# Optimization experiments

Measured on AMD Instinct MI355X. Metric: run time of the kernel, lower is better.

## Reference

```python
import jax, jax.numpy as jnp
import numpy as np

B, C, H, W = 4, 32, 512, 512


def _warp_add(x, flow, residual):
    # x: [B,C,H,W], flow: [B,2,H,W], residual: [B,C,H,W]
    Bs, Cs, Hs, Ws = x.shape
    # align_corners=False pixel-center base grid in [-1,1]
    gy = (jnp.arange(Hs, dtype=x.dtype) + 0.5) * (2.0 / Hs) - 1.0  # [H]
    gx = (jnp.arange(Ws, dtype=x.dtype) + 0.5) * (2.0 / Ws) - 1.0  # [W]
    grid_x = gx[None, None, :] + flow[:, 0]  # [B,H,W]
    grid_y = gy[None, :, None] + flow[:, 1]  # [B,H,W]
    # circular wrap on x only
    grid_x = jnp.mod(grid_x + 1.0, 2.0) - 1.0
    real_x = (grid_x + 1.0) * (Ws * 0.5) - 0.5
    real_y = (grid_y + 1.0) * (Hs * 0.5) - 0.5
    x0 = jnp.floor(real_x)
    y0 = jnp.floor(real_y)
    dx = real_x - x0
    dy = real_y - y0
    ix0 = x0.astype(jnp.int32)
    iy0 = y0.astype(jnp.int32)
    ix1 = ix0 + 1
    iy1 = iy0 + 1

    def valid(ix, iy):
        return (ix >= 0) & (ix < Ws) & (iy >= 0) & (iy < Hs)

    xf = x.reshape(Bs, Cs, Hs * Ws)

    def gather(ix, iy):
        v = valid(ix, iy)  # [B,H,W]
        idx = jnp.clip(iy, 0, Hs - 1) * Ws + jnp.clip(ix, 0, Ws - 1)  # [B,H,W]
        g = jnp.take_along_axis(xf, idx.reshape(Bs, 1, Hs * Ws), axis=2)  # [B,C,H*W]
        g = g.reshape(Bs, Cs, Hs, Ws)
        return jnp.where(v[:, None, :, :], g, 0.0)

    v_tl = gather(ix0, iy0)
    v_tr = gather(ix1, iy0)
    v_bl = gather(ix0, iy1)
    v_br = gather(ix1, iy1)

    w_tl = ((1.0 - dx) * (1.0 - dy))[:, None]
    w_tr = (dx * (1.0 - dy))[:, None]
    w_bl = ((1.0 - dx) * dy)[:, None]
    w_br = (dx * dy)[:, None]

    out = w_tl * v_tl + w_tr * v_tr + w_bl * v_bl + w_br * v_br + residual
    return out


def setup_inputs() -> dict:
    key = jax.random.key(0)
    k1, k2, k3 = jax.random.split(key, 3)
    x = jax.random.normal(k1, (B, C, H, W), dtype=jnp.float32)
    flow = jax.random.normal(k2, (B, 2, H, W), dtype=jnp.float32) * 0.1
    residual = jax.random.normal(k3, (B, C, H, W), dtype=jnp.float32)
    return {"x": x, "flow": flow, "residual": residual}


def reference(x, flow, residual):
    return _warp_add(x, flow, residual)
```

## Files before the change

### kernel.cpp

```cpp
#include <hip/hip_runtime.h>

#define Bdim 4
#define Cdim 32
#define Hdim 512
#define Wdim 512
#define HWdim (Hdim * Wdim)

typedef __attribute__((ext_vector_type(2))) float    f32x2;
typedef __attribute__((ext_vector_type(4))) float    f32x4;
typedef __attribute__((ext_vector_type(2))) _Float16 f16x2;
typedef __attribute__((ext_vector_type(4))) _Float16 f16x4;
typedef __attribute__((ext_vector_type(8))) _Float16 f16x8;

__global__ __launch_bounds__(256) void transpose_nhwc_half_kernel(
    const float* __restrict__ x, _Float16* __restrict__ ws)
{
    __shared__ float lds[Cdim * 65];

    const int idx = blockIdx.x;
    const int tw  = idx & 7;
    const int h   = (idx >> 3) & (Hdim - 1);
    const int b   = idx >> 12;
    const int w0  = tw * 64;

    const int t  = threadIdx.x;
    const int wi = t & 63;
    const int cg = t >> 6;

    #pragma unroll
    for (int i = 0; i < 8; ++i) {
        const int c = cg * 8 + i;
        lds[c * 65 + wi] = x[(((size_t)b * Cdim + c) * Hdim + h) * Wdim + w0 + wi];
    }
    __syncthreads();

    const size_t base = (((size_t)b * Hdim + h) * Wdim + w0) * Cdim;
    const int w_ = t >> 2;
    const int c0 = (t & 3) * 8;
    f16x8 v;
    #pragma unroll
    for (int k = 0; k < 8; ++k) v[k] = (_Float16)lds[(c0 + k) * 65 + w_];
    *(f16x8*)(ws + base + (size_t)t * 8) = v;
}

__global__ __launch_bounds__(256) void gather_nhwc_half_kernel(
    const _Float16* __restrict__ ws,
    const float* __restrict__ flow,
    const float* __restrict__ residual,
    float* __restrict__ out)
{
    __shared__ int      s_off[4][256];
    __shared__ float    s_wt[4][256];
    __shared__ _Float16 s_buf[256 * 34];

    const int idx = blockIdx.x;
    const int b   = idx >> 10;
    const int h   = (idx >> 1) & (Hdim - 1);
    const int w0  = (idx & 1) << 8;
    const int t   = threadIdx.x;

    {
        const int w = w0 + t;
        const int pixg = h * Wdim + w;
        const float fx = flow[((size_t)b * 2 + 0) * HWdim + pixg];
        const float fy = flow[((size_t)b * 2 + 1) * HWdim + pixg];

        float gx = ((float)w + 0.5f) * (2.0f / (float)Wdim) - 1.0f + fx;
        float gy = ((float)h + 0.5f) * (2.0f / (float)Hdim) - 1.0f + fy;

        float tm = fmodf(gx + 1.0f, 2.0f);
        if (tm < 0.0f) tm += 2.0f;
        gx = tm - 1.0f;

        const float real_x = (gx + 1.0f) * ((float)Wdim * 0.5f) - 0.5f;
        const float real_y = (gy + 1.0f) * ((float)Hdim * 0.5f) - 0.5f;

        const float x0f = floorf(real_x);
        const float y0f = floorf(real_y);
        const float dx = real_x - x0f;
        const float dy = real_y - y0f;

        const int ix0 = (int)x0f;
        const int iy0 = (int)y0f;
        const int ix1 = ix0 + 1;
        const int iy1 = iy0 + 1;

        const bool vx0 = (ix0 >= 0) && (ix0 < Wdim);
        const bool vx1 = (ix1 >= 0) && (ix1 < Wdim);
        const bool vy0 = (iy0 >= 0) && (iy0 < Hdim);
        const bool vy1 = (iy1 >= 0) && (iy1 < Hdim);

        const int cx0 = min(max(ix0, 0), Wdim - 1);
        const int cx1 = min(max(ix1, 0), Wdim - 1);
        const int cy0 = min(max(iy0, 0), Hdim - 1);
        const int cy1 = min(max(iy1, 0), Hdim - 1);

        float w_tl = (1.0f - dx) * (1.0f - dy);
        float w_tr = dx * (1.0f - dy);
        float w_bl = (1.0f - dx) * dy;
        float w_br = dx * dy;
        if (!(vx0 && vy0)) w_tl = 0.0f;
        if (!(vx1 && vy0)) w_tr = 0.0f;
        if (!(vx0 && vy1)) w_bl = 0.0f;
        if (!(vx1 && vy1)) w_br = 0.0f;

        s_off[0][t] = (cy0 * Wdim + cx0) * Cdim;
        s_off[1][t] = (cy0 * Wdim + cx1) * Cdim;
        s_off[2][t] = (cy1 * Wdim + cx0) * Cdim;
        s_off[3][t] = (cy1 * Wdim + cx1) * Cdim;
        s_wt[0][t] = w_tl;
        s_wt[1][t] = w_tr;
        s_wt[2][t] = w_bl;
        s_wt[3][t] = w_br;
    }
    __syncthreads();

    {
        const int ci = t & 7;
        const int c0 = ci * 4;
        const int p  = t >> 3;
        const _Float16* xb = ws + (size_t)b * HWdim * Cdim + c0;

        #pragma unroll 4
        for (int j = 0; j < 8; ++j) {
            const int pix = j * 32 + p;
            const int o0 = s_off[0][pix];
            const int o1 = s_off[1][pix];
            const int o2 = s_off[2][pix];
            const int o3 = s_off[3][pix];
            const float w0_ = s_wt[0][pix];
            const float w1_ = s_wt[1][pix];
            const float w2_ = s_wt[2][pix];
            const float w3_ = s_wt[3][pix];

            const f16x4 v0 = *(const f16x4*)(xb + o0);
            const f16x4 v1 = *(const f16x4*)(xb + o1);
            const f16x4 v2 = *(const f16x4*)(xb + o2);
            const f16x4 v3 = *(const f16x4*)(xb + o3);

            float a0 = w0_ * (float)v0[0] + w1_ * (float)v1[0] + w2_ * (float)v2[0] + w3_ * (float)v3[0];
            float a1 = w0_ * (float)v0[1] + w1_ * (float)v1[1] + w2_ * (float)v2[1] + w3_ * (float)v3[1];
            float a2 = w0_ * (float)v0[2] + w1_ * (float)v1[2] + w2_ * (float)v2[2] + w3_ * (float)v3[2];
            float a3 = w0_ * (float)v0[3] + w1_ * (float)v1[3] + w2_ * (float)v2[3] + w3_ * (float)v3[3];

            f16x2 h01; h01[0] = (_Float16)a0; h01[1] = (_Float16)a1;
            f16x2 h23; h23[0] = (_Float16)a2; h23[1] = (_Float16)a3;
            *(f16x2*)(s_buf + pix * 34 + c0)     = h01;
            *(f16x2*)(s_buf + pix * 34 + c0 + 2) = h23;
        }
    }
    __syncthreads();

    {
        const size_t pbase = (size_t)h * Wdim + w0 + t;
        const _Float16* row = s_buf + t * 34;
        #pragma unroll 8
        for (int cc = 0; cc < Cdim; cc += 2) {
            const f16x2 v = *(const f16x2*)(row + cc);
            const size_t gi0 = ((size_t)b * Cdim + cc) * HWdim + pbase;
            const float r0 = __builtin_nontemporal_load(residual + gi0);
            const float r1 = __builtin_nontemporal_load(residual + gi0 + HWdim);
            __builtin_nontemporal_store((float)v[0] + r0, out + gi0);
            __builtin_nontemporal_store((float)v[1] + r1, out + gi0 + HWdim);
        }
    }
}

__global__ __launch_bounds__(256) void warp_add_kernel(
    const float* __restrict__ x,
    const float* __restrict__ flow,
    const float* __restrict__ residual,
    float* __restrict__ out)
{
    int tid = blockIdx.x * blockDim.x + threadIdx.x;
    int w = tid & (Wdim - 1);
    int h = (tid >> 9) & (Hdim - 1);
    int b = tid >> 18;

    const float fx = flow[((size_t)b * 2 + 0) * HWdim + h * Wdim + w];
    const float fy = flow[((size_t)b * 2 + 1) * HWdim + h * Wdim + w];

    float gx = ((float)w + 0.5f) * (2.0f / (float)Wdim) - 1.0f + fx;
    float gy = ((float)h + 0.5f) * (2.0f / (float)Hdim) - 1.0f + fy;
    {
        float t2 = fmodf(gx + 1.0f, 2.0f);
        if (t2 < 0.0f) t2 += 2.0f;
        gx = t2 - 1.0f;
    }
    const float real_x = (gx + 1.0f) * ((float)Wdim * 0.5f) - 0.5f;
    const float real_y = (gy + 1.0f) * ((float)Hdim * 0.5f) - 0.5f;
    const float x0f = floorf(real_x);
    const float y0f = floorf(real_y);
    const float dx = real_x - x0f;
    const float dy = real_y - y0f;
    const int ix0 = (int)x0f, iy0 = (int)y0f;
    const int ix1 = ix0 + 1,  iy1 = iy0 + 1;
    const bool vx0 = (ix0 >= 0) && (ix0 < Wdim);
    const bool vx1 = (ix1 >= 0) && (ix1 < Wdim);
    const bool vy0 = (iy0 >= 0) && (iy0 < Hdim);
    const bool vy1 = (iy1 >= 0) && (iy1 < Hdim);
    const int cx0 = min(max(ix0, 0), Wdim - 1);
    const int cx1 = min(max(ix1, 0), Wdim - 1);
    const int cy0 = min(max(iy0, 0), Hdim - 1);
    const int cy1 = min(max(iy1, 0), Hdim - 1);
    float w_tl = (1.0f - dx) * (1.0f - dy);
    float w_tr = dx * (1.0f - dy);
    float w_bl = (1.0f - dx) * dy;
    float w_br = dx * dy;
    if (!(vx0 && vy0)) w_tl = 0.0f;
    if (!(vx1 && vy0)) w_tr = 0.0f;
    if (!(vx0 && vy1)) w_bl = 0.0f;
    if (!(vx1 && vy1)) w_br = 0.0f;
    const int off_tl = cy0 * Wdim + cx0;
    const int off_tr = cy0 * Wdim + cx1;
    const int off_bl = cy1 * Wdim + cx0;
    const int off_br = cy1 * Wdim + cx1;
    const size_t base = (size_t)b * Cdim * HWdim;
    const int    pix  = h * Wdim + w;
    const float* xb = x + base;
    const float* rb = residual + base + pix;
    float*       ob = out + base + pix;
    #pragma unroll 8
    for (int c = 0; c < Cdim; ++c) {
        const float* xc = xb + (size_t)c * HWdim;
        float v = w_tl * xc[off_tl] + w_tr * xc[off_tr]
                + w_bl * xc[off_bl] + w_br * xc[off_br]
                + rb[(size_t)c * HWdim];
        ob[(size_t)c * HWdim] = v;
    }
}

extern "C" void kernel_launch(void* const* d_in, const int* in_sizes, int n_in,
                              void* d_out, int out_size, void* d_ws, size_t ws_size,
                              hipStream_t stream) {
    const float* x        = (const float*)d_in[0];
    const float* flow     = (const float*)d_in[1];
    const float* residual = (const float*)d_in[2];
    float* out            = (float*)d_out;

    const size_t ws_needed = (size_t)Bdim * Cdim * HWdim * sizeof(_Float16);

    if (ws_size >= ws_needed) {
        _Float16* ws = (_Float16*)d_ws;
        transpose_nhwc_half_kernel<<<Bdim * Hdim * (Wdim / 64), 256, 0, stream>>>(x, ws);
        gather_nhwc_half_kernel<<<Bdim * Hdim * Wdim / 256, 256, 0, stream>>>(ws, flow, residual, out);
    } else {
        const int total = Bdim * Hdim * Wdim;
        warp_add_kernel<<<total / 256, 256, 0, stream>>>(x, flow, residual, out);
    }
}
```

Measured before the change: 349.2 us.

## Widen transpose tiles and batch gather loads with early residual prefetch

The transpose kernel now handles 128-wide tiles and uses float4 global loads, writing two f16x8 chunks per thread. The gather kernel gives each thread 8 channels with f16x8 loads and issues all bilinear corner loads for two pixel batches up front. It also prefetches all 32 residual values into registers before the interpolation math, so gather and residual reads overlap. The cost is much higher register pressure, up to 32 residual floats plus 16 vector loads in flight, which may reduce occupancy.

```diff
diff --git a/kernel.cpp b/kernel.cpp
--- a/kernel.cpp
+++ b/kernel.cpp
@@ -6,7 +6,6 @@
 #define Wdim 512
 #define HWdim (Hdim * Wdim)
 
-typedef __attribute__((ext_vector_type(2))) float    f32x2;
 typedef __attribute__((ext_vector_type(4))) float    f32x4;
 typedef __attribute__((ext_vector_type(2))) _Float16 f16x2;
 typedef __attribute__((ext_vector_type(4))) _Float16 f16x4;
@@ -15,32 +14,40 @@
 __global__ __launch_bounds__(256) void transpose_nhwc_half_kernel(
     const float* __restrict__ x, _Float16* __restrict__ ws)
 {
-    __shared__ float lds[Cdim * 65];
+    __shared__ float lds[Cdim * 132];
 
     const int idx = blockIdx.x;
-    const int tw  = idx & 7;
-    const int h   = (idx >> 3) & (Hdim - 1);
-    const int b   = idx >> 12;
-    const int w0  = tw * 64;
-
-    const int t  = threadIdx.x;
-    const int wi = t & 63;
-    const int cg = t >> 6;
-
-    #pragma unroll
-    for (int i = 0; i < 8; ++i) {
-        const int c = cg * 8 + i;
-        lds[c * 65 + wi] = x[(((size_t)b * Cdim + c) * Hdim + h) * Wdim + w0 + wi];
+    const int tw  = idx & 3;
+    const int h   = (idx >> 2) & (Hdim - 1);
+    const int b   = idx >> 11;
+    const int w0  = tw * 128;
+    const int t   = threadIdx.x;
+
+    f32x4 r[4];
+    #pragma unroll
+    for (int i = 0; i < 4; ++i) {
+        const int f4 = i * 256 + t;
+        const int c  = f4 >> 5;
+        const int w4 = f4 & 31;
+        r[i] = *(const f32x4*)(x + (((size_t)b * Cdim + c) * Hdim + h) * Wdim + w0 + w4 * 4);
+    }
+    #pragma unroll
+    for (int i = 0; i < 4; ++i) {
+        const int f4 = i * 256 + t;
+        *(f32x4*)(lds + (f4 >> 5) * 132 + (f4 & 31) * 4) = r[i];
     }
     __syncthreads();
 
     const size_t base = (((size_t)b * Hdim + h) * Wdim + w0) * Cdim;
-    const int w_ = t >> 2;
-    const int c0 = (t & 3) * 8;
-    f16x8 v;
-    #pragma unroll
-    for (int k = 0; k < 8; ++k) v[k] = (_Float16)lds[(c0 + k) * 65 + w_];
-    *(f16x8*)(ws + base + (size_t)t * 8) = v;
+    const int w_ = t >> 1;
+    const int c0 = (t & 1) * 16;
+    f16x8 v0, v1;
+    #pragma unroll
+    for (int k = 0; k < 8; ++k) v0[k] = (_Float16)lds[(c0 + k) * 132 + w_];
+    #pragma unroll
+    for (int k = 0; k < 8; ++k) v1[k] = (_Float16)lds[(c0 + 8 + k) * 132 + w_];
+    *(f16x8*)(ws + base + (size_t)w_ * Cdim + c0)     = v0;
+    *(f16x8*)(ws + base + (size_t)w_ * Cdim + c0 + 8) = v1;
 }
 
 __global__ __launch_bounds__(256) void gather_nhwc_half_kernel(
@@ -51,7 +58,7 @@
 {
     __shared__ int      s_off[4][256];
     __shared__ float    s_wt[4][256];
-    __shared__ _Float16 s_buf[256 * 34];
+    __shared__ _Float16 s_buf[256 * 36];
 
     const int idx = blockIdx.x;
     const int b   = idx >> 10;
@@ -115,53 +122,83 @@
     }
     __syncthreads();
 
+    const int ci = t & 3;
+    const int c0 = ci * 8;
+    const int p  = t >> 2;
+    const _Float16* xb = ws + (size_t)b * (size_t)HWdim * Cdim + c0;
+    const size_t pbase = (size_t)h * Wdim + w0 + t;
+    const float* rb = residual + (size_t)b * Cdim * (size_t)HWdim + pbase;
+
+    float rres[Cdim];
+
+    int   oa[2][4]; float wa[2][4]; f16x8 va[2][4];
+    #pragma unroll
+    for (int j = 0; j < 2; ++j) {
+        const int pix = j * 64 + p;
+        #pragma unroll
+        for (int k = 0; k < 4; ++k) { oa[j][k] = s_off[k][pix]; wa[j][k] = s_wt[k][pix]; }
+    }
+    #pragma unroll
+    for (int j = 0; j < 2; ++j) {
+        #pragma unroll
+        for (int k = 0; k < 4; ++k) va[j][k] = *(const f16x8*)(xb + (size_t)oa[j][k]);
+    }
+    #pragma unroll
+    for (int c = 0; c < Cdim; ++c) rres[c] = __builtin_nontemporal_load(rb + (size_t)c * HWdim);
+
+    #pragma unroll
+    for (int j = 0; j < 2; ++j) {
+        const int pix = j * 64 + p;
+        float acc[8];
+        #pragma unroll
+        for (int e = 0; e < 8; ++e)
+            acc[e] = wa[j][0] * (float)va[j][0][e] + wa[j][1] * (float)va[j][1][e]
+                   + wa[j][2] * (float)va[j][2][e] + wa[j][3] * (float)va[j][3][e];
+        f16x4 h0, h1;
+        #pragma unroll
+        for (int e = 0; e < 4; ++e) { h0[e] = (_Float16)acc[e]; h1[e] = (_Float16)acc[4 + e]; }
+        *(f16x4*)(s_buf + pix * 36 + c0)     = h0;
+        *(f16x4*)(s_buf + pix * 36 + c0 + 4) = h1;
+    }
+
+    int   ob[2][4]; float wb[2][4]; f16x8 vb[2][4];
+    #pragma unroll
+    for (int j = 0; j < 2; ++j) {
+        const int pix = 128 + j * 64 + p;
+        #pragma unroll
+        for (int k = 0; k < 4; ++k) { ob[j][k] = s_off[k][pix]; wb[j][k] = s_wt[k][pix]; }
+    }
+    #pragma unroll
+    for (int j = 0; j < 2; ++j) {
+        #pragma unroll
+        for (int k = 0; k < 4; ++k) vb[j][k] = *(const f16x8*)(xb + (size_t)ob[j][k]);
+    }
+    #pragma unroll
+    for (int j = 0; j < 2; ++j) {
+        const int pix = 128 + j * 64 + p;
+        float acc[8];
+        #pragma unroll
+        for (int e = 0; e < 8; ++e)
+            acc[e] = wb[j][0] * (float)vb[j][0][e] + wb[j][1] * (float)vb[j][1][e]
+                   + wb[j][2] * (float)vb[j][2][e] + wb[j][3] * (float)vb[j][3][e];
+        f16x4 h0, h1;
+        #pragma unroll
+        for (int e = 0; e < 4; ++e) { h0[e] = (_Float16)acc[e]; h1[e] = (_Float16)acc[4 + e]; }
+        *(f16x4*)(s_buf + pix * 36 + c0)     = h0;
+        *(f16x4*)(s_buf + pix * 36 + c0 + 4) = h1;
+    }
+    __syncthreads();
+
     {
-        const int ci = t & 7;
-        const int c0 = ci * 4;
-        const int p  = t >> 3;
-        const _Float16* xb = ws + (size_t)b * HWdim * Cdim + c0;
-
-        #pragma unroll 4
-        for (int j = 0; j < 8; ++j) {
-            const int pix = j * 32 + p;
-            const int o0 = s_off[0][pix];
-            const int o1 = s_off[1][pix];
-            const int o2 = s_off[2][pix];
-            const int o3 = s_off[3][pix];
-            const float w0_ = s_wt[0][pix];
-            const float w1_ = s_wt[1][pix];
-            const float w2_ = s_wt[2][pix];
-            const float w3_ = s_wt[3][pix];
-
-            const f16x4 v0 = *(const f16x4*)(xb + o0);
-            const f16x4 v1 = *(const f16x4*)(xb + o1);
-            const f16x4 v2 = *(const f16x4*)(xb + o2);
-            const f16x4 v3 = *(const f16x4*)(xb + o3);
-
-            float a0 = w0_ * (float)v0[0] + w1_ * (float)v1[0] + w2_ * (float)v2[0] + w3_ * (float)v3[0];
-            float a1 = w0_ * (float)v0[1] + w1_ * (float)v1[1] + w2_ * (float)v2[1] + w3_ * (float)v3[1];
-            float a2 = w0_ * (float)v0[2] + w1_ * (float)v1[2] + w2_ * (float)v2[2] + w3_ * (float)v3[2];
-            float a3 = w0_ * (float)v0[3] + w1_ * (float)v1[3] + w2_ * (float)v2[3] + w3_ * (float)v3[3];
-
-            f16x2 h01; h01[0] = (_Float16)a0; h01[1] = (_Float16)a1;
-            f16x2 h23; h23[0] = (_Float16)a2; h23[1] = (_Float16)a3;
-            *(f16x2*)(s_buf + pix * 34 + c0)     = h01;
-            *(f16x2*)(s_buf + pix * 34 + c0 + 2) = h23;
-        }
-    }
-    __syncthreads();
-
-    {
-        const size_t pbase = (size_t)h * Wdim + w0 + t;
-        const _Float16* row = s_buf + t * 34;
-        #pragma unroll 8
-        for (int cc = 0; cc < Cdim; cc += 2) {
-            const f16x2 v = *(const f16x2*)(row + cc);
-            const size_t gi0 = ((size_t)b * Cdim + cc) * HWdim + pbase;
-            const float r0 = __builtin_nontemporal_load(residual + gi0);
-            const float r1 = __builtin_nontemporal_load(residual + gi0 + HWdim);
-            __builtin_nontemporal_store((float)v[0] + r0, out + gi0);
-            __builtin_nontemporal_store((float)v[1] + r1, out + gi0 + HWdim);
+        const size_t obase = (size_t)b * Cdim * (size_t)HWdim + pbase;
+        const _Float16* row = s_buf + t * 36;
+        #pragma unroll
+        for (int cc = 0; cc < Cdim; cc += 4) {
+            const f16x4 v = *(const f16x4*)(row + cc);
+            #pragma unroll
+            for (int e = 0; e < 4; ++e)
+                __builtin_nontemporal_store((float)v[e] + rres[cc + e],
+                                            out + obase + (size_t)(cc + e) * HWdim);
         }
     }
 }
@@ -218,14 +255,14 @@
     const size_t base = (size_t)b * Cdim * HWdim;
     const int    pix  = h * Wdim + w;
     const float* xb = x + base;
-    const float* rb = residual + base + pix;
+    const float* rbp = residual + base + pix;
     float*       ob = out + base + pix;
     #pragma unroll 8
     for (int c = 0; c < Cdim; ++c) {
         const float* xc = xb + (size_t)c * HWdim;
         float v = w_tl * xc[off_tl] + w_tr * xc[off_tr]
                 + w_bl * xc[off_bl] + w_br * xc[off_br]
-                + rb[(size_t)c * HWdim];
+                + rbp[(size_t)c * HWdim];
         ob[(size_t)c * HWdim] = v;
     }
 }
@@ -242,7 +279,7 @@
 
     if (ws_size >= ws_needed) {
         _Float16* ws = (_Float16*)d_ws;
-        transpose_nhwc_half_kernel<<<Bdim * Hdim * (Wdim / 64), 256, 0, stream>>>(x, ws);
+        transpose_nhwc_half_kernel<<<Bdim * Hdim * (Wdim / 128), 256, 0, stream>>>(x, ws);
         gather_nhwc_half_kernel<<<Bdim * Hdim * Wdim / 256, 256, 0, stream>>>(ws, flow, residual, out);
     } else {
         const int total = Bdim * Hdim * Wdim;
```

Measured after the change: 352.6 us. About the same (+0.9%).

## Vectorize transpose loads and write gather output directly without LDS staging

Applied to the files above, without the earlier changes.

The transpose kernel now handles 128-wide tiles and loads x with float4 vector reads, then writes two f16x8 chunks per thread. The gather kernel drops the shared-memory staging buffer and second sync. Each thread now reads residual and writes output directly for its 4 channels, and the per-pixel stores across p are contiguous within each channel. This removes the LDS round trip and half-precision requantization of the interpolated value. The trade-off is that stores are now strided across channels per thread, which may hurt coalescing compared with the old per-pixel channel loop.

```diff
diff --git a/kernel.cpp b/kernel.cpp
--- a/kernel.cpp
+++ b/kernel.cpp
@@ -6,7 +6,6 @@
 #define Wdim 512
 #define HWdim (Hdim * Wdim)
 
-typedef __attribute__((ext_vector_type(2))) float    f32x2;
 typedef __attribute__((ext_vector_type(4))) float    f32x4;
 typedef __attribute__((ext_vector_type(2))) _Float16 f16x2;
 typedef __attribute__((ext_vector_type(4))) _Float16 f16x4;
@@ -15,32 +14,40 @@
 __global__ __launch_bounds__(256) void transpose_nhwc_half_kernel(
     const float* __restrict__ x, _Float16* __restrict__ ws)
 {
-    __shared__ float lds[Cdim * 65];
+    __shared__ float lds[Cdim * 132];
 
     const int idx = blockIdx.x;
-    const int tw  = idx & 7;
-    const int h   = (idx >> 3) & (Hdim - 1);
-    const int b   = idx >> 12;
-    const int w0  = tw * 64;
-
-    const int t  = threadIdx.x;
-    const int wi = t & 63;
-    const int cg = t >> 6;
-
-    #pragma unroll
-    for (int i = 0; i < 8; ++i) {
-        const int c = cg * 8 + i;
-        lds[c * 65 + wi] = x[(((size_t)b * Cdim + c) * Hdim + h) * Wdim + w0 + wi];
+    const int tw  = idx & 3;
+    const int h   = (idx >> 2) & (Hdim - 1);
+    const int b   = idx >> 11;
+    const int w0  = tw * 128;
+    const int t   = threadIdx.x;
+
+    f32x4 r[4];
+    #pragma unroll
+    for (int i = 0; i < 4; ++i) {
+        const int f4 = i * 256 + t;
+        const int c  = f4 >> 5;
+        const int w4 = f4 & 31;
+        r[i] = *(const f32x4*)(x + (((size_t)b * Cdim + c) * Hdim + h) * Wdim + w0 + w4 * 4);
+    }
+    #pragma unroll
+    for (int i = 0; i < 4; ++i) {
+        const int f4 = i * 256 + t;
+        *(f32x4*)(lds + (f4 >> 5) * 132 + (f4 & 31) * 4) = r[i];
     }
     __syncthreads();
 
     const size_t base = (((size_t)b * Hdim + h) * Wdim + w0) * Cdim;
-    const int w_ = t >> 2;
-    const int c0 = (t & 3) * 8;
-    f16x8 v;
-    #pragma unroll
-    for (int k = 0; k < 8; ++k) v[k] = (_Float16)lds[(c0 + k) * 65 + w_];
-    *(f16x8*)(ws + base + (size_t)t * 8) = v;
+    const int w_ = t >> 1;
+    const int c0 = (t & 1) * 16;
+    f16x8 v0, v1;
+    #pragma unroll
+    for (int k = 0; k < 8; ++k) v0[k] = (_Float16)lds[(c0 + k) * 132 + w_];
+    #pragma unroll
+    for (int k = 0; k < 8; ++k) v1[k] = (_Float16)lds[(c0 + 8 + k) * 132 + w_];
+    *(f16x8*)(ws + base + (size_t)w_ * Cdim + c0)     = v0;
+    *(f16x8*)(ws + base + (size_t)w_ * Cdim + c0 + 8) = v1;
 }
 
 __global__ __launch_bounds__(256) void gather_nhwc_half_kernel(
@@ -49,9 +56,8 @@
     const float* __restrict__ residual,
     float* __restrict__ out)
 {
-    __shared__ int      s_off[4][256];
-    __shared__ float    s_wt[4][256];
-    __shared__ _Float16 s_buf[256 * 34];
+    __shared__ int   s_off[4][256];
+    __shared__ float s_wt[4][256];
 
     const int idx = blockIdx.x;
     const int b   = idx >> 10;
@@ -119,7 +125,9 @@
         const int ci = t & 7;
         const int c0 = ci * 4;
         const int p  = t >> 3;
-        const _Float16* xb = ws + (size_t)b * HWdim * Cdim + c0;
+        const _Float16* xb = ws + (size_t)b * (size_t)HWdim * Cdim + c0;
+        const size_t gbase = ((size_t)b * Cdim + c0) * (size_t)HWdim
+                           + (size_t)h * Wdim + w0;
 
         #pragma unroll 4
         for (int j = 0; j < 8; ++j) {
@@ -138,30 +146,21 @@
             const f16x4 v2 = *(const f16x4*)(xb + o2);
             const f16x4 v3 = *(const f16x4*)(xb + o3);
 
-            float a0 = w0_ * (float)v0[0] + w1_ * (float)v1[0] + w2_ * (float)v2[0] + w3_ * (float)v3[0];
-            float a1 = w0_ * (float)v0[1] + w1_ * (float)v1[1] + w2_ * (float)v2[1] + w3_ * (float)v3[1];
-            float a2 = w0_ * (float)v0[2] + w1_ * (float)v1[2] + w2_ * (float)v2[2] + w3_ * (float)v3[2];
-            float a3 = w0_ * (float)v0[3] + w1_ * (float)v1[3] + w2_ * (float)v2[3] + w3_ * (float)v3[3];
-
-            f16x2 h01; h01[0] = (_Float16)a0; h01[1] = (_Float16)a1;
-            f16x2 h23; h23[0] = (_Float16)a2; h23[1] = (_Float16)a3;
-            *(f16x2*)(s_buf + pix * 34 + c0)     = h01;
-            *(f16x2*)(s_buf + pix * 34 + c0 + 2) = h23;
-        }
-    }
-    __syncthreads();
-
-    {
-        const size_t pbase = (size_t)h * Wdim + w0 + t;
-        const _Float16* row = s_buf + t * 34;
-        #pragma unroll 8
-        for (int cc = 0; cc < Cdim; cc += 2) {
-            const f16x2 v = *(const f16x2*)(row + cc);
-            const size_t gi0 = ((size_t)b * Cdim + cc) * HWdim + pbase;
-            const float r0 = __builtin_nontemporal_load(residual + gi0);
-            const float r1 = __builtin_nontemporal_load(residual + gi0 + HWdim);
-            __builtin_nontemporal_store((float)v[0] + r0, out + gi0);
-            __builtin_nontemporal_store((float)v[1] + r1, out + gi0 + HWdim);
+            const size_t gi = gbase + (size_t)pix;
+            const float r0 = __builtin_nontemporal_load(residual + gi);
+            const float r1 = __builtin_nontemporal_load(residual + gi + (size_t)HWdim);
+            const float r2 = __builtin_nontemporal_load(residual + gi + (size_t)(2 * HWdim));
+            const float r3 = __builtin_nontemporal_load(residual + gi + (size_t)(3 * HWdim));
+
+            const float a0 = w0_ * (float)v0[0] + w1_ * (float)v1[0] + w2_ * (float)v2[0] + w3_ * (float)v3[0];
+            const float a1 = w0_ * (float)v0[1] + w1_ * (float)v1[1] + w2_ * (float)v2[1] + w3_ * (float)v3[1];
+            const float a2 = w0_ * (float)v0[2] + w1_ * (float)v1[2] + w2_ * (float)v2[2] + w3_ * (float)v3[2];
+            const float a3 = w0_ * (float)v0[3] + w1_ * (float)v1[3] + w2_ * (float)v2[3] + w3_ * (float)v3[3];
+
+            __builtin_nontemporal_store(a0 + r0, out + gi);
+            __builtin_nontemporal_store(a1 + r1, out + gi + (size_t)HWdim);
+            __builtin_nontemporal_store(a2 + r2, out + gi + (size_t)(2 * HWdim));
+            __builtin_nontemporal_store(a3 + r3, out + gi + (size_t)(3 * HWdim));
         }
     }
 }
@@ -218,14 +217,14 @@
     const size_t base = (size_t)b * Cdim * HWdim;
     const int    pix  = h * Wdim + w;
     const float* xb = x + base;
-    const float* rb = residual + base + pix;
+    const float* rbp = residual + base + pix;
     float*       ob = out + base + pix;
     #pragma unroll 8
     for (int c = 0; c < Cdim; ++c) {
         const float* xc = xb + (size_t)c * HWdim;
         float v = w_tl * xc[off_tl] + w_tr * xc[off_tr]
                 + w_bl * xc[off_bl] + w_br * xc[off_br]
-                + rb[(size_t)c * HWdim];
+                + rbp[(size_t)c * HWdim];
         ob[(size_t)c * HWdim] = v;
     }
 }
@@ -242,7 +241,7 @@
 
     if (ws_size >= ws_needed) {
         _Float16* ws = (_Float16*)d_ws;
-        transpose_nhwc_half_kernel<<<Bdim * Hdim * (Wdim / 64), 256, 0, stream>>>(x, ws);
+        transpose_nhwc_half_kernel<<<Bdim * Hdim * (Wdim / 128), 256, 0, stream>>>(x, ws);
         gather_nhwc_half_kernel<<<Bdim * Hdim * Wdim / 256, 256, 0, stream>>>(ws, flow, residual, out);
     } else {
         const int total = Bdim * Hdim * Wdim;
```

Result: slower. 489.5 us (+40.2%).
